# Kernel tuning notes

Measured on AMD Instinct MI355X. Metric: run time of the kernel, lower is better.

Reference implementation:

```python
import jax, jax.numpy as jnp
import numpy as np

B, S, D, H, L, F = 2, 2048, 512, 8, 6, 2048
MAX = 5000
HD = D // H
OFF = MAX - 1


def _layernorm(x, g, b, eps=1e-5):
    m = jnp.mean(x, axis=-1, keepdims=True)
    v = jnp.mean((x - m) ** 2, axis=-1, keepdims=True)
    return (x - m) / jnp.sqrt(v + eps) * g + b


def _sinusoidal_pe(seq_len, d_model):
    pos = jnp.arange(seq_len, dtype=jnp.float32)[:, None]
    div = jnp.exp(jnp.arange(0, d_model, 2, dtype=jnp.float32) * (-np.log(10000.0) / d_model))
    pe = jnp.zeros((seq_len, d_model), jnp.float32)
    pe = pe.at[:, 0::2].set(jnp.sin(pos * div))
    pe = pe.at[:, 1::2].set(jnp.cos(pos * div))
    return pe


def setup_inputs() -> dict:
    key = jax.random.key(0)
    ks = iter(jax.random.split(key, 64))

    def n(shape, s):
        return (jax.random.normal(next(ks), shape, jnp.float32) * s).astype(jnp.float32)

    inp = {}
    inp['x'] = jax.random.normal(next(ks), (B, S, D), jnp.float32)
    inp['f0'] = jax.random.normal(next(ks), (B, S, 1), jnp.float32)
    inp['sp'] = jax.random.normal(next(ks), (B, S, 1), jnp.float32)
    inp['ap'] = jax.random.normal(next(ks), (B, S, 1), jnp.float32)
    inp['spk_emb'] = jax.random.normal(next(ks), (B, D), jnp.float32)
    # conditional positional encoding projections (weights stored as (in,out); y = x @ W + b)
    inp['Wf0'] = n((1, D), 0.1); inp['bf0'] = jnp.zeros((D,), jnp.float32)
    inp['Wsp'] = n((1, D), 0.1); inp['bsp'] = jnp.zeros((D,), jnp.float32)
    inp['Wap'] = n((1, D), 0.1); inp['bap'] = jnp.zeros((D,), jnp.float32)
    inp['Wspk'] = n((D, D), 0.02); inp['bspk'] = jnp.zeros((D,), jnp.float32)
    # per-layer stacked params
    inp['Wq'] = n((L, D, D), 0.02); inp['bq'] = jnp.zeros((L, D), jnp.float32)
    inp['Wk'] = n((L, D, D), 0.02); inp['bk'] = jnp.zeros((L, D), jnp.float32)
    inp['Wv'] = n((L, D, D), 0.02); inp['bv'] = jnp.zeros((L, D), jnp.float32)
    inp['Wo'] = n((L, D, D), 0.02); inp['bo'] = jnp.zeros((L, D), jnp.float32)
    inp['ln1_g'] = jnp.ones((L, D), jnp.float32); inp['ln1_b'] = jnp.zeros((L, D), jnp.float32)
    inp['ln2_g'] = jnp.ones((L, D), jnp.float32); inp['ln2_b'] = jnp.zeros((L, D), jnp.float32)
    inp['W1'] = n((L, D, F), 0.02); inp['b1'] = jnp.zeros((L, F), jnp.float32)
    inp['W2'] = n((L, F, D), 0.02); inp['b2'] = jnp.zeros((L, D), jnp.float32)
    inp['rel_table'] = n((L, 2 * MAX - 1, H), 0.02)
    inp['gfin'] = jnp.ones((D,), jnp.float32); inp['bfin'] = jnp.zeros((D,), jnp.float32)
    return inp


def _forward(x, f0, sp, ap, spk_emb,
             Wf0, bf0, Wsp, bsp, Wap, bap, Wspk, bspk,
             Wq, bq, Wk, bk, Wv, bv, Wo, bo,
             ln1_g, ln1_b, ln2_g, ln2_b, W1, b1, W2, b2,
             rel_table, gfin, bfin):
    # --- conditional positional encoding (dropout = identity, eval mode) ---
    x = x + _sinusoidal_pe(S, D)[None]
    x = x + (f0 @ Wf0 + bf0)
    x = x + (sp @ Wsp + bsp)
    x = x + (ap @ Wap + bap)
    spk = jnp.broadcast_to(spk_emb[:, None, :], (B, S, D))
    x = x + (spk @ Wspk + bspk)

    # relative coords: added bias for (query q, key k) is table[k - q + OFF] (matches transpose(1,3) in torch)
    coords = jnp.arange(S)
    rel = jnp.clip(coords[None, :] - coords[:, None] + OFF, 0, 2 * MAX - 2)  # (S_q, S_k)

    scale = 1.0 / np.sqrt(HD)

    def layer(x, p):
        (Wq_, bq_, Wk_, bk_, Wv_, bv_, Wo_, bo_,
         g1, be1, g2, be2, W1_, b1_, W2_, b2_, tab) = p
        res = x
        h = _layernorm(x, g1, be1)
        Q = (h @ Wq_ + bq_).reshape(B, S, H, HD)
        K = (h @ Wk_ + bk_).reshape(B, S, H, HD)
        V = (h @ Wv_ + bv_).reshape(B, S, H, HD)
        scores = jnp.einsum('bqhd,bkhd->bhqk', Q, K) * scale
        bias = jnp.transpose(tab[rel], (2, 0, 1))  # (H, S_q, S_k)
        scores = scores + bias[None]
        attn = jax.nn.softmax(scores, axis=-1)
        ao = jnp.einsum('bhqk,bkhd->bqhd', attn, V).reshape(B, S, D)
        x = res + (ao @ Wo_ + bo_)
        res = x
        h = _layernorm(x, g2, be2)
        h = jax.nn.gelu(h @ W1_ + b1_, approximate=False)
        x = res + (h @ W2_ + b2_)
        return x, None

    params = (Wq, bq, Wk, bk, Wv, bv, Wo, bo,
              ln1_g, ln1_b, ln2_g, ln2_b, W1, b1, W2, b2, rel_table)
    x, _ = jax.lax.scan(layer, x, params)
    return _layernorm(x, gfin, bfin)


def reference(x, f0, sp, ap, spk_emb,
              Wf0, bf0, Wsp, bsp, Wap, bap, Wspk, bspk,
              Wq, bq, Wk, bk, Wv, bv, Wo, bo,
              ln1_g, ln1_b, ln2_g, ln2_b, W1, b1, W2, b2,
              rel_table, gfin, bfin):
    return _forward(x, f0, sp, ap, spk_emb,
                    Wf0, bf0, Wsp, bsp, Wap, bap, Wspk, bspk,
                    Wq, bq, Wk, bk, Wv, bv, Wo, bo,
                    ln1_g, ln1_b, ln2_g, ln2_b, W1, b1, W2, b2,
                    rel_table, gfin, bfin)
```

## Files before the change

kernel.cpp:

```cpp
#include <hip/hip_runtime.h>
#include <hip/hip_bf16.h>

#define B_ 2
#define S_ 2048
#define D_ 512
#define H_ 8
#define L_ 6
#define F_ 2048
#define HD_ 64
#define M_ 4096
#define OFF_ 4999
#define NREL_ 9999

typedef short s8v __attribute__((ext_vector_type(8)));
typedef float f4v __attribute__((ext_vector_type(4)));

enum { MODE_BF16 = 0, MODE_RES = 1, MODE_GELU = 2 };

__device__ __forceinline__ short f2bf(float f) {
  unsigned u = __float_as_uint(f);
  unsigned r = (u + 0x7fffu + ((u >> 16) & 1u)) >> 16;
  return (short)r;
}

__device__ __forceinline__ float exp2fast(float x) {
  float r;
  asm("v_exp_f32 %0, %1" : "=v"(r) : "v"(x));
  return r;
}

__device__ __forceinline__ void gload16(const void* g, const void* l) {
  __builtin_amdgcn_global_load_lds((const __attribute__((address_space(1))) unsigned int*)g,
                                   (__attribute__((address_space(3))) unsigned int*)l,
                                   16, 0, 0);
}

__global__ void transpose_kernel(const float* __restrict__ src, short* __restrict__ dst,
                                 int K, int N, long srcBS, long dstBS, int rowOff)
{
  __shared__ float t[32][33];
  int tx = threadIdx.x, ty = threadIdx.y;
  int n0 = blockIdx.x * 32, k0 = blockIdx.y * 32, l = blockIdx.z;
  const float* s = src + (size_t)l * srcBS;
  short* d = dst + (size_t)l * dstBS;
  for (int j = 0; j < 4; ++j)
    t[ty + j*8][tx] = s[(size_t)(k0 + ty + j*8) * N + n0 + tx];
  __syncthreads();
  for (int j = 0; j < 4; ++j)
    d[(size_t)(rowOff + n0 + ty + j*8) * K + k0 + tx] = f2bf(t[tx][ty + j*8]);
}

__global__ void packb_kernel(const float* __restrict__ bq, const float* __restrict__ bk,
                             const float* __restrict__ bv, float* __restrict__ bqkv)
{
  int i = blockIdx.x * 256 + threadIdx.x;
  if (i >= L_ * 1536) return;
  int l = i / 1536, j = i % 1536;
  float v = (j < 512) ? bq[l*512 + j] : (j < 1024) ? bk[l*512 + j - 512] : bv[l*512 + j - 1024];
  bqkv[i] = v;
}

__global__ void tabt_kernel(const float* __restrict__ tab, float* __restrict__ tabT)
{
  int i = blockIdx.x * 256 + threadIdx.x;
  if (i >= L_ * H_ * NREL_) return;
  int l = i / (H_ * NREL_), rem = i % (H_ * NREL_);
  int h = rem / NREL_, idx = rem % NREL_;
  tabT[i] = tab[((size_t)l * NREL_ + idx) * H_ + h] * 1.44269504f;
}

__global__ __launch_bounds__(256) void spk_kernel(const float* __restrict__ spk,
                                                  const float* __restrict__ Wspk,
                                                  const float* __restrict__ bspk,
                                                  float* __restrict__ sproj)
{
  __shared__ float red[4][64];
  int b = blockIdx.x, nb = blockIdx.y;
  int dl = threadIdx.x & 63, kc = threadIdx.x >> 6;
  int d = nb * 64 + dl;
  const float* sprow = spk + b * D_;
  float a0 = 0.f, a1 = 0.f;
  int kbeg = kc * 128;
  for (int k = kbeg; k < kbeg + 128; k += 2) {
    a0 += sprow[k]     * Wspk[(size_t)k * D_ + d];
    a1 += sprow[k + 1] * Wspk[(size_t)(k + 1) * D_ + d];
  }
  red[kc][dl] = a0 + a1;
  __syncthreads();
  if (kc == 0)
    sproj[b*D_ + d] = red[0][dl] + red[1][dl] + red[2][dl] + red[3][dl] + bspk[d];
}

__global__ __launch_bounds__(256) void prologue_kernel(
    const float* __restrict__ x, const float* __restrict__ f0, const float* __restrict__ sp,
    const float* __restrict__ ap, const float* __restrict__ Wf0, const float* __restrict__ bf0,
    const float* __restrict__ Wsp, const float* __restrict__ bsp,
    const float* __restrict__ Wap, const float* __restrict__ bap,
    const float* __restrict__ sproj, float* __restrict__ X)
{
  int row = blockIdx.x, tid = threadIdx.x;
  int b = row >> 11, s = row & 2047;
  float vf0 = f0[row], vsp = sp[row], vap = ap[row];
  for (int j = 0; j < 2; ++j) {
    int d = tid + j * 256;
    int i = d >> 1;
    float div = expf((float)(2*i) * -0.01798894603f);
    float arg = (float)s * div;
    float pe = (d & 1) ? cosf(arg) : sinf(arg);
    float v = x[(size_t)row*D_ + d] + pe
            + vf0*Wf0[d] + bf0[d] + vsp*Wsp[d] + bsp[d] + vap*Wap[d] + bap[d]
            + sproj[b*D_ + d];
    X[(size_t)row*D_ + d] = v;
  }
}

__global__ __launch_bounds__(256) void ln_kernel(
    const float* __restrict__ X, const float* __restrict__ g, const float* __restrict__ bta,
    short* __restrict__ outB, float* __restrict__ outF, int f32out)
{
  __shared__ float red[8];
  int row = blockIdx.x, tid = threadIdx.x;
  const float* xr = X + (size_t)row * D_;
  float v0 = xr[tid], v1 = xr[tid + 256];
  float s = v0 + v1, q = v0*v0 + v1*v1;
  for (int off = 1; off < 64; off <<= 1) { s += __shfl_xor(s, off); q += __shfl_xor(q, off); }
  int w = tid >> 6;
  if ((tid & 63) == 0) { red[w*2] = s; red[w*2 + 1] = q; }
  __syncthreads();
  s = red[0] + red[2] + red[4] + red[6];
  q = red[1] + red[3] + red[5] + red[7];
  float mean = s * (1.0f / D_);
  float var = q * (1.0f / D_) - mean * mean;
  float rstd = rsqrtf(var + 1e-5f);
  float o0 = (v0 - mean) * rstd * g[tid] + bta[tid];
  float o1 = (v1 - mean) * rstd * g[tid + 256] + bta[tid + 256];
  if (f32out) {
    outF[(size_t)row*D_ + tid] = o0; outF[(size_t)row*D_ + tid + 256] = o1;
  } else {
    outB[(size_t)row*D_ + tid] = f2bf(o0); outB[(size_t)row*D_ + tid + 256] = f2bf(o1);
  }
}

template<int MODE>
__device__ __forceinline__ void gemm_body(
    const short* __restrict__ A, const short* __restrict__ Wt,
    const float* __restrict__ bias, int K, int N,
    float* outF, short* outB)
{
  __shared__ short sA[2][4096];
  __shared__ short sB[2][2048];
  const int tid = threadIdx.x;
  const int w = tid >> 6, lane = tid & 63;
  const int col = lane & 15, quad = lane >> 4;
  const int m0 = blockIdx.x * 128, n0 = blockIdx.y * 64;
  const int z = blockIdx.z;
  const int Ksub = K / gridDim.z;
  const int kbase = z * Ksub;
  const int nkt = Ksub >> 6;

  const int rowT = tid >> 2, kcA = tid & 3;
  const size_t kc8 = kcA * 8;

  f4v acc[2][4] = {};
  for (int kt = 0; kt < nkt; ++kt) {
    const int k0 = kbase + kt * 64;
    __syncthreads();
    for (int p = 0; p < 2; ++p) {
      gload16(A + (size_t)(m0 + rowT) * K + k0 + p*32 + kc8,       &sA[p][(w*16) * 32]);
      gload16(A + (size_t)(m0 + 64 + rowT) * K + k0 + p*32 + kc8,  &sA[p][(64 + w*16) * 32]);
      gload16(Wt + (size_t)(n0 + rowT) * K + k0 + p*32 + kc8,      &sB[p][(w*16) * 32]);
    }
    __syncthreads();
    for (int p = 0; p < 2; ++p) {
      s8v af[2], bfr[4];
      for (int mt = 0; mt < 2; ++mt)
        af[mt] = *(const s8v*)&sA[p][(w*32 + mt*16 + col) * 32 + quad * 8];
      for (int nt = 0; nt < 4; ++nt)
        bfr[nt] = *(const s8v*)&sB[p][(nt*16 + col) * 32 + quad * 8];
      for (int mt = 0; mt < 2; ++mt)
        for (int nt = 0; nt < 4; ++nt)
          acc[mt][nt] = __builtin_amdgcn_mfma_f32_16x16x32_bf16(af[mt], bfr[nt], acc[mt][nt], 0, 0, 0);
    }
  }

  const float qsc = (MODE == MODE_BF16 && n0 < 512) ? 0.18033688f : 1.0f;
  float bz[4];
  for (int nt = 0; nt < 4; ++nt)
    bz[nt] = (z == 0) ? bias[n0 + nt*16 + col] : 0.0f;
  for (int mt = 0; mt < 2; ++mt) {
    int mbase = m0 + w*32 + mt*16 + quad*4;
    for (int nt = 0; nt < 4; ++nt) {
      int n = n0 + nt*16 + col;
      for (int r = 0; r < 4; ++r) {
        float v = acc[mt][nt][r] + bz[nt];
        size_t idx = (size_t)(mbase + r) * N + n;
        if (MODE == MODE_RES) {
          atomicAdd(outF + idx, v);
        } else if (MODE == MODE_GELU) {
          outB[idx] = f2bf(0.5f * v * (1.0f + erff(v * 0.70710678118f)));
        } else {
          outB[idx] = f2bf(v * qsc);
        }
      }
    }
  }
}

__global__ __launch_bounds__(256) void gemm_qkv_kernel(
    const short* __restrict__ A, const short* __restrict__ Wt,
    const float* __restrict__ bias, float* outF, short* outB)
{ gemm_body<MODE_BF16>(A, Wt, bias, 512, 1536, outF, outB); }

__global__ __launch_bounds__(256) void gemm_o_kernel(
    const short* __restrict__ A, const short* __restrict__ Wt,
    const float* __restrict__ bias, float* outF, short* outB)
{ gemm_body<MODE_RES>(A, Wt, bias, 512, 512, outF, outB); }

__global__ __launch_bounds__(256) void gemm_ffn1_kernel(
    const short* __restrict__ A, const short* __restrict__ Wt,
    const float* __restrict__ bias, float* outF, short* outB)
{ gemm_body<MODE_GELU>(A, Wt, bias, 512, 2048, outF, outB); }

__global__ __launch_bounds__(256) void gemm_ffn2_kernel(
    const short* __restrict__ A, const short* __restrict__ Wt,
    const float* __restrict__ bias, float* outF, short* outB)
{ gemm_body<MODE_RES>(A, Wt, bias, 2048, 512, outF, outB); }

__global__ __launch_bounds__(256) void vtrans_kernel(const short* __restrict__ QKV,
                                                     short* __restrict__ Vt)
{
  __shared__ short t[64 * 72];
  int tid = threadIdx.x;
  int s0 = blockIdx.x * 64, bh = blockIdx.y;
  int b = bh >> 3, h = bh & 7;
  for (int it = 0; it < 2; ++it) {
    int c = it * 256 + tid;
    int sR = c >> 3, hc = c & 7;
    s8v v = *(const s8v*)(QKV + (size_t)(b*S_ + s0 + sR) * 1536 + 1024 + h*64 + hc*8);
    *(s8v*)&t[sR * 72 + hc * 8] = v;
  }
  __syncthreads();
  for (int it = 0; it < 2; ++it) {
    int c = it * 256 + tid;
    int hd = c >> 3, sc = c & 7;
    s8v v;
    for (int j = 0; j < 8; ++j) v[j] = t[(sc*8 + j) * 72 + hd];
    *(s8v*)(Vt + (size_t)(bh*64 + hd) * S_ + s0 + sc*8) = v;
  }
}

__global__ __launch_bounds__(512) void flash_kernel(
    const short* __restrict__ QKV, const short* __restrict__ Vt,
    const float* __restrict__ tabT, short* __restrict__ AO)
{
  __shared__ __attribute__((aligned(16))) short sQ[2 * 128 * 40];
  __shared__ __attribute__((aligned(16))) short sK[2 * 2 * 32 * 40];
  __shared__ __attribute__((aligned(16))) short sV[2 * 64 * 40];
  __shared__ __attribute__((aligned(16))) short sP[8 * 2 * 16 * 40];
  __shared__ float sBias[192];
  __shared__ float sRow[8 * 16];

  const int tid = threadIdx.x;
  const int w = tid >> 6, lane = tid & 63;
  const int col = lane & 15, quad = lane >> 4;
  const int bh = blockIdx.x, qt = blockIdx.y;
  const int b = bh >> 3, h = bh & 7;
  const int q0 = qt * 128;
  const int wq = w * 16;
  const int nkt = S_ / 64;
  const float* tabh = tabT + (size_t)h * NREL_;

  for (int j = 0; j < 2; ++j) {
    int Lc = j * 512 + tid;
    int c4q = Lc & 3, q = (Lc >> 2) & 127, hc = Lc >> 9;
    *(int4*)&sQ[hc*5120 + q*40 + c4q*8] =
      *(const int4*)(QKV + (size_t)(b*S_ + q0 + q) * 1536 + h*64 + hc*32 + c4q*8);
  }

  const int c4 = tid & 3;
  const int kK = (tid >> 2) & 63, hcK = tid >> 8;
  const short* gK = QKV + (size_t)(b*S_ + kK) * 1536 + 512 + h*64 + hcK*32 + c4*8;
  short* dK = &sK[(kK >> 5)*2560 + hcK*1280 + (kK & 31)*40 + c4*8];
  const int c8 = tid & 7, hdV = tid >> 3;
  const short* gV = Vt + (size_t)(bh*64 + hdV) * S_ + c8*8;
  short* dV = &sV[(c8 >> 2)*2560 + hdV*40 + (c8 & 3)*8];

  int4 rk = *(const int4*)gK;
  int4 rv = *(const int4*)gV;
  float rbias = (tid < 192) ? tabh[0 - q0 - 127 + OFF_ + tid] : 0.0f;

  s8v bQ[2];
  float lsum = 0.0f;
  f4v o[4] = {};

  for (int kt = 0; kt < nkt; ++kt) {
    __syncthreads();
    *(int4*)dK = rk;
    *(int4*)dV = rv;
    if (tid < 192) sBias[tid] = rbias;
    __syncthreads();
    if (kt == 0) {
      bQ[0] = *(const s8v*)&sQ[0*5120 + (wq + col)*40 + quad*8];
      bQ[1] = *(const s8v*)&sQ[1*5120 + (wq + col)*40 + quad*8];
    }
    if (kt + 1 < nkt) {
      rk = *(const int4*)(gK + (size_t)(kt + 1) * 64 * 1536);
      rv = *(const int4*)(gV + (kt + 1) * 64);
      if (tid < 192) rbias = tabh[(kt + 1)*64 - q0 - 127 + OFF_ + tid];
    }

    for (int ko = 0; ko < 2; ++ko) {
      f4v st[2] = {};
      for (int mt = 0; mt < 2; ++mt) {
        s8v aK0 = *(const s8v*)&sK[ko*2560 + 0*1280 + (mt*16 + col)*40 + quad*8];
        s8v aK1 = *(const s8v*)&sK[ko*2560 + 1*1280 + (mt*16 + col)*40 + quad*8];
        st[mt] = __builtin_amdgcn_mfma_f32_16x16x32_bf16(aK0, bQ[0], st[mt], 0, 0, 0);
        st[mt] = __builtin_amdgcn_mfma_f32_16x16x32_bf16(aK1, bQ[1], st[mt], 0, 0, 0);
      }
      for (int mt = 0; mt < 2; ++mt) {
        int ib0 = ko*32 + mt*16 + quad*4 + 127 - wq - col;
        float p0 = exp2fast(st[mt][0] + sBias[ib0 + 0]);
        float p1 = exp2fast(st[mt][1] + sBias[ib0 + 1]);
        float p2 = exp2fast(st[mt][2] + sBias[ib0 + 2]);
        float p3 = exp2fast(st[mt][3] + sBias[ib0 + 3]);
        lsum += (p0 + p1) + (p2 + p3);
        unsigned u0 = __float_as_uint(p0) + 0x8000u;
        unsigned u1 = __float_as_uint(p1) + 0x8000u;
        unsigned u2 = __float_as_uint(p2) + 0x8000u;
        unsigned u3 = __float_as_uint(p3) + 0x8000u;
        int2 pk;
        pk.x = (int)((u0 >> 16) | (u1 & 0xffff0000u));
        pk.y = (int)((u2 >> 16) | (u3 & 0xffff0000u));
        *(int2*)&sP[w*1280 + ko*640 + col*40 + mt*16 + quad*4] = pk;
      }
      s8v aP = *(const s8v*)&sP[w*1280 + ko*640 + col*40 + quad*8];
      for (int nt = 0; nt < 4; ++nt) {
        s8v bv = *(const s8v*)&sV[ko*2560 + (nt*16 + col)*40 + quad*8];
        o[nt] = __builtin_amdgcn_mfma_f32_16x16x32_bf16(aP, bv, o[nt], 0, 0, 0);
      }
    }
  }

  lsum += __shfl_xor(lsum, 16);
  lsum += __shfl_xor(lsum, 32);
  if (lane < 16) sRow[w*16 + lane] = lsum;
  float rs[4];
  for (int r = 0; r < 4; ++r) rs[r] = sRow[w*16 + quad*4 + r];
  for (int nt = 0; nt < 4; ++nt)
    for (int r = 0; r < 4; ++r) {
      float v = o[nt][r] / rs[r];
      size_t m = (size_t)(b*S_ + q0 + wq + quad*4 + r);
      AO[m * 512 + h*64 + nt*16 + col] = f2bf(v);
    }
}

extern "C" void kernel_launch(void* const* d_in, const int* in_sizes, int n_in,
                              void* d_out, int out_size, void* d_ws, size_t ws_size,
                              hipStream_t stream)
{
  const float* x    = (const float*)d_in[0];
  const float* f0   = (const float*)d_in[1];
  const float* sp   = (const float*)d_in[2];
  const float* ap   = (const float*)d_in[3];
  const float* spk  = (const float*)d_in[4];
  const float* Wf0  = (const float*)d_in[5];  const float* bf0  = (const float*)d_in[6];
  const float* Wsp  = (const float*)d_in[7];  const float* bsp  = (const float*)d_in[8];
  const float* Wap  = (const float*)d_in[9];  const float* bap  = (const float*)d_in[10];
  const float* Wspk = (const float*)d_in[11]; const float* bspk = (const float*)d_in[12];
  const float* Wq   = (const float*)d_in[13]; const float* bq   = (const float*)d_in[14];
  const float* Wk   = (const float*)d_in[15]; const float* bk   = (const float*)d_in[16];
  const float* Wv   = (const float*)d_in[17]; const float* bv   = (const float*)d_in[18];
  const float* Wo   = (const float*)d_in[19]; const float* bo   = (const float*)d_in[20];
  const float* ln1g = (const float*)d_in[21]; const float* ln1b = (const float*)d_in[22];
  const float* ln2g = (const float*)d_in[23]; const float* ln2b = (const float*)d_in[24];
  const float* W1   = (const float*)d_in[25]; const float* b1   = (const float*)d_in[26];
  const float* W2   = (const float*)d_in[27]; const float* b2   = (const float*)d_in[28];
  const float* tab  = (const float*)d_in[29];
  const float* gfin = (const float*)d_in[30]; const float* bfin = (const float*)d_in[31];

  char* p = (char*)d_ws;
  auto alloc = [&](size_t bytes) { char* r = p; p += (bytes + 255) & ~(size_t)255; return r; };
  short* WqkvT = (short*)alloc((size_t)L_ * 1536 * 512 * 2);
  short* WoT   = (short*)alloc((size_t)L_ * 512 * 512 * 2);
  short* W1T   = (short*)alloc((size_t)L_ * 2048 * 512 * 2);
  short* W2T   = (short*)alloc((size_t)L_ * 512 * 2048 * 2);
  float* bqkv  = (float*)alloc((size_t)L_ * 1536 * 4);
  float* X     = (float*)alloc((size_t)M_ * D_ * 4);
  short* Hb    = (short*)alloc((size_t)M_ * D_ * 2);
  short* AO    = (short*)alloc((size_t)M_ * D_ * 2);
  short* QKVb  = (short*)alloc((size_t)M_ * 1536 * 2);
  short* VtG   = (short*)alloc((size_t)B_ * H_ * HD_ * S_ * 2);
  short* H1b   = QKVb;
  float* sproj = (float*)alloc((size_t)B_ * D_ * 4);
  float* tabT  = (float*)alloc((size_t)L_ * H_ * NREL_ * 4);

  dim3 b256(256);
  dim3 tb(32, 8);
  packb_kernel<<<dim3((L_*1536 + 255)/256), b256, 0, stream>>>(bq, bk, bv, bqkv);
  tabt_kernel<<<dim3((L_*H_*NREL_ + 255)/256), b256, 0, stream>>>(tab, tabT);
  transpose_kernel<<<dim3(16, 16, L_), tb, 0, stream>>>(Wq, WqkvT, 512, 512, 512*512, 1536*512, 0);
  transpose_kernel<<<dim3(16, 16, L_), tb, 0, stream>>>(Wk, WqkvT, 512, 512, 512*512, 1536*512, 512);
  transpose_kernel<<<dim3(16, 16, L_), tb, 0, stream>>>(Wv, WqkvT, 512, 512, 512*512, 1536*512, 1024);
  transpose_kernel<<<dim3(16, 16, L_), tb, 0, stream>>>(Wo, WoT, 512, 512, 512*512, 512*512, 0);
  transpose_kernel<<<dim3(64, 16, L_), tb, 0, stream>>>(W1, W1T, 512, 2048, 512*2048, 2048*512, 0);
  transpose_kernel<<<dim3(16, 64, L_), tb, 0, stream>>>(W2, W2T, 2048, 512, 2048*512, 512*2048, 0);
  spk_kernel<<<dim3(B_, 8), b256, 0, stream>>>(spk, Wspk, bspk, sproj);
  prologue_kernel<<<dim3(M_), b256, 0, stream>>>(x, f0, sp, ap, Wf0, bf0, Wsp, bsp, Wap, bap, sproj, X);

  for (int l = 0; l < L_; ++l) {
    ln_kernel<<<dim3(M_), b256, 0, stream>>>(X, ln1g + l*D_, ln1b + l*D_, Hb, nullptr, 0);
    gemm_qkv_kernel<<<dim3(32, 24, 1), b256, 0, stream>>>(
        Hb, WqkvT + (size_t)l*1536*512, bqkv + l*1536, nullptr, QKVb);
    vtrans_kernel<<<dim3(S_/64, B_*H_), b256, 0, stream>>>(QKVb, VtG);
    flash_kernel<<<dim3(B_*H_, S_/128), dim3(512), 0, stream>>>(QKVb, VtG, tabT + (size_t)l*H_*NREL_, AO);
    gemm_o_kernel<<<dim3(32, 8, 2), b256, 0, stream>>>(
        AO, WoT + (size_t)l*512*512, bo + l*D_, X, nullptr);
    ln_kernel<<<dim3(M_), b256, 0, stream>>>(X, ln2g + l*D_, ln2b + l*D_, Hb, nullptr, 0);
    gemm_ffn1_kernel<<<dim3(32, 32, 1), b256, 0, stream>>>(
        Hb, W1T + (size_t)l*2048*512, b1 + l*F_, nullptr, H1b);
    gemm_ffn2_kernel<<<dim3(32, 8, 4), b256, 0, stream>>>(
        H1b, W2T + (size_t)l*512*2048, b2 + l*D_, X, nullptr);
  }
  ln_kernel<<<dim3(M_), b256, 0, stream>>>(X, gfin, bfin, nullptr, (float*)d_out, 1);
}
```

Baseline: 1.019 ms.

## Split attention over two key halves and fuse V transpose into QKV GEMM

The flash attention grid gains a z dimension that splits the key sequence in two. Each half writes unnormalized bf16 partial outputs and row sums, and a new combine kernel adds them and normalizes. This doubles the block count so the GPU is better filled. The QKV GEMM epilogue now writes V directly in transposed per-head layout, which removes the separate vtrans kernel and its pass over memory. In exchange it adds the combine kernel, extra partial-output traffic and bf16 rounding of the unnormalized partials.

```diff
diff --git a/kernel.cpp b/kernel.cpp
--- a/kernel.cpp
+++ b/kernel.cpp
@@ -21,6 +21,10 @@
   unsigned u = __float_as_uint(f);
   unsigned r = (u + 0x7fffu + ((u >> 16) & 1u)) >> 16;
   return (short)r;
+}
+
+__device__ __forceinline__ float bf2f(short s) {
+  return __uint_as_float(((unsigned)(unsigned short)s) << 16);
 }
 
 __device__ __forceinline__ float exp2fast(float x) {
@@ -145,7 +149,7 @@
 __device__ __forceinline__ void gemm_body(
     const short* __restrict__ A, const short* __restrict__ Wt,
     const float* __restrict__ bias, int K, int N,
-    float* outF, short* outB)
+    float* outF, short* outB, short* outV)
 {
   __shared__ short sA[2][4096];
   __shared__ short sB[2][2048];
@@ -189,6 +193,20 @@
     bz[nt] = (z == 0) ? bias[n0 + nt*16 + col] : 0.0f;
   for (int mt = 0; mt < 2; ++mt) {
     int mbase = m0 + w*32 + mt*16 + quad*4;
+    if (MODE == MODE_BF16 && n0 >= 1024) {
+      int bb = mbase >> 11, ss = mbase & 2047;
+      for (int nt = 0; nt < 4; ++nt) {
+        int hn = n0 + nt*16 + col - 1024;
+        int hh = hn >> 6, hd = hn & 63;
+        short4 pv;
+        pv.x = f2bf(acc[mt][nt][0] + bz[nt]);
+        pv.y = f2bf(acc[mt][nt][1] + bz[nt]);
+        pv.z = f2bf(acc[mt][nt][2] + bz[nt]);
+        pv.w = f2bf(acc[mt][nt][3] + bz[nt]);
+        *(short4*)(outV + ((size_t)((bb << 3) + hh) * 64 + hd) * S_ + ss) = pv;
+      }
+      continue;
+    }
     for (int nt = 0; nt < 4; ++nt) {
       int n = n0 + nt*16 + col;
       for (int r = 0; r < 4; ++r) {
@@ -208,66 +226,44 @@
 
 __global__ __launch_bounds__(256) void gemm_qkv_kernel(
     const short* __restrict__ A, const short* __restrict__ Wt,
-    const float* __restrict__ bias, float* outF, short* outB)
-{ gemm_body<MODE_BF16>(A, Wt, bias, 512, 1536, outF, outB); }
+    const float* __restrict__ bias, float* outF, short* outB, short* outV)
+{ gemm_body<MODE_BF16>(A, Wt, bias, 512, 1536, outF, outB, outV); }
 
 __global__ __launch_bounds__(256) void gemm_o_kernel(
     const short* __restrict__ A, const short* __restrict__ Wt,
     const float* __restrict__ bias, float* outF, short* outB)
-{ gemm_body<MODE_RES>(A, Wt, bias, 512, 512, outF, outB); }
+{ gemm_body<MODE_RES>(A, Wt, bias, 512, 512, outF, outB, nullptr); }
 
 __global__ __launch_bounds__(256) void gemm_ffn1_kernel(
     const short* __restrict__ A, const short* __restrict__ Wt,
     const float* __restrict__ bias, float* outF, short* outB)
-{ gemm_body<MODE_GELU>(A, Wt, bias, 512, 2048, outF, outB); }
+{ gemm_body<MODE_GELU>(A, Wt, bias, 512, 2048, outF, outB, nullptr); }
 
 __global__ __launch_bounds__(256) void gemm_ffn2_kernel(
     const short* __restrict__ A, const short* __restrict__ Wt,
     const float* __restrict__ bias, float* outF, short* outB)
-{ gemm_body<MODE_RES>(A, Wt, bias, 2048, 512, outF, outB); }
-
-__global__ __launch_bounds__(256) void vtrans_kernel(const short* __restrict__ QKV,
-                                                     short* __restrict__ Vt)
-{
-  __shared__ short t[64 * 72];
-  int tid = threadIdx.x;
-  int s0 = blockIdx.x * 64, bh = blockIdx.y;
-  int b = bh >> 3, h = bh & 7;
-  for (int it = 0; it < 2; ++it) {
-    int c = it * 256 + tid;
-    int sR = c >> 3, hc = c & 7;
-    s8v v = *(const s8v*)(QKV + (size_t)(b*S_ + s0 + sR) * 1536 + 1024 + h*64 + hc*8);
-    *(s8v*)&t[sR * 72 + hc * 8] = v;
-  }
-  __syncthreads();
-  for (int it = 0; it < 2; ++it) {
-    int c = it * 256 + tid;
-    int hd = c >> 3, sc = c & 7;
-    s8v v;
-    for (int j = 0; j < 8; ++j) v[j] = t[(sc*8 + j) * 72 + hd];
-    *(s8v*)(Vt + (size_t)(bh*64 + hd) * S_ + s0 + sc*8) = v;
-  }
-}
+{ gemm_body<MODE_RES>(A, Wt, bias, 2048, 512, outF, outB, nullptr); }
 
 __global__ __launch_bounds__(512) void flash_kernel(
     const short* __restrict__ QKV, const short* __restrict__ Vt,
-    const float* __restrict__ tabT, short* __restrict__ AO)
+    const float* __restrict__ tabT, short* __restrict__ OP,
+    float* __restrict__ lsumB)
 {
   __shared__ __attribute__((aligned(16))) short sQ[2 * 128 * 40];
   __shared__ __attribute__((aligned(16))) short sK[2 * 2 * 32 * 40];
   __shared__ __attribute__((aligned(16))) short sV[2 * 64 * 40];
   __shared__ __attribute__((aligned(16))) short sP[8 * 2 * 16 * 40];
   __shared__ float sBias[192];
-  __shared__ float sRow[8 * 16];
 
   const int tid = threadIdx.x;
   const int w = tid >> 6, lane = tid & 63;
   const int col = lane & 15, quad = lane >> 4;
-  const int bh = blockIdx.x, qt = blockIdx.y;
+  const int bh = blockIdx.x, qt = blockIdx.y, z = blockIdx.z;
   const int b = bh >> 3, h = bh & 7;
   const int q0 = qt * 128;
+  const int KB = z * (S_ / 2);
   const int wq = w * 16;
-  const int nkt = S_ / 64;
+  const int nkt = S_ / 128;
   const float* tabh = tabT + (size_t)h * NREL_;
 
   for (int j = 0; j < 2; ++j) {
@@ -279,15 +275,15 @@
 
   const int c4 = tid & 3;
   const int kK = (tid >> 2) & 63, hcK = tid >> 8;
-  const short* gK = QKV + (size_t)(b*S_ + kK) * 1536 + 512 + h*64 + hcK*32 + c4*8;
+  const short* gK = QKV + (size_t)(b*S_ + KB + kK) * 1536 + 512 + h*64 + hcK*32 + c4*8;
   short* dK = &sK[(kK >> 5)*2560 + hcK*1280 + (kK & 31)*40 + c4*8];
   const int c8 = tid & 7, hdV = tid >> 3;
-  const short* gV = Vt + (size_t)(bh*64 + hdV) * S_ + c8*8;
+  const short* gV = Vt + (size_t)(bh*64 + hdV) * S_ + KB + c8*8;
   short* dV = &sV[(c8 >> 2)*2560 + hdV*40 + (c8 & 3)*8];
 
   int4 rk = *(const int4*)gK;
   int4 rv = *(const int4*)gV;
-  float rbias = (tid < 192) ? tabh[0 - q0 - 127 + OFF_ + tid] : 0.0f;
+  float rbias = (tid < 192) ? tabh[KB + 0 - q0 - 127 + OFF_ + tid] : 0.0f;
 
   s8v bQ[2];
   float lsum = 0.0f;
@@ -306,7 +302,7 @@
     if (kt + 1 < nkt) {
       rk = *(const int4*)(gK + (size_t)(kt + 1) * 64 * 1536);
       rv = *(const int4*)(gV + (kt + 1) * 64);
-      if (tid < 192) rbias = tabh[(kt + 1)*64 - q0 - 127 + OFF_ + tid];
+      if (tid < 192) rbias = tabh[KB + (kt + 1)*64 - q0 - 127 + OFF_ + tid];
     }
 
     for (int ko = 0; ko < 2; ++ko) {
@@ -343,15 +339,29 @@
 
   lsum += __shfl_xor(lsum, 16);
   lsum += __shfl_xor(lsum, 32);
-  if (lane < 16) sRow[w*16 + lane] = lsum;
-  float rs[4];
-  for (int r = 0; r < 4; ++r) rs[r] = sRow[w*16 + quad*4 + r];
+  if (lane < 16)
+    lsumB[(size_t)z * (B_*H_*S_) + (size_t)bh * S_ + q0 + wq + lane] = lsum;
+  short* op = OP + (size_t)z * M_ * 512;
   for (int nt = 0; nt < 4; ++nt)
     for (int r = 0; r < 4; ++r) {
-      float v = o[nt][r] / rs[r];
       size_t m = (size_t)(b*S_ + q0 + wq + quad*4 + r);
-      AO[m * 512 + h*64 + nt*16 + col] = f2bf(v);
-    }
+      op[m * 512 + h*64 + nt*16 + col] = f2bf(o[nt][r]);
+    }
+}
+
+__global__ __launch_bounds__(256) void ocomb_kernel(
+    const short* __restrict__ OP, const float* __restrict__ lsumB,
+    short* __restrict__ AO)
+{
+  int m = blockIdx.x, tid = threadIdx.x;
+  int b = m >> 11, s = m & 2047;
+  for (int j = 0; j < 2; ++j) {
+    int d = tid + j * 256;
+    int bh = (b << 3) + (d >> 6);
+    float l = lsumB[(size_t)bh * S_ + s] + lsumB[(size_t)(B_*H_*S_) + (size_t)bh * S_ + s];
+    float o = bf2f(OP[(size_t)m * 512 + d]) + bf2f(OP[(size_t)(M_ + m) * 512 + d]);
+    AO[(size_t)m * 512 + d] = f2bf(o / l);
+  }
 }
 
 extern "C" void kernel_launch(void* const* d_in, const int* in_sizes, int n_in,
@@ -393,6 +403,8 @@
   short* H1b   = QKVb;
   float* sproj = (float*)alloc((size_t)B_ * D_ * 4);
   float* tabT  = (float*)alloc((size_t)L_ * H_ * NREL_ * 4);
+  short* OP    = (short*)alloc((size_t)2 * M_ * 512 * 2);
+  float* lsumB = (float*)alloc((size_t)2 * B_ * H_ * S_ * 4);
 
   dim3 b256(256);
   dim3 tb(32, 8);
@@ -410,9 +422,10 @@
   for (int l = 0; l < L_; ++l) {
     ln_kernel<<<dim3(M_), b256, 0, stream>>>(X, ln1g + l*D_, ln1b + l*D_, Hb, nullptr, 0);
     gemm_qkv_kernel<<<dim3(32, 24, 1), b256, 0, stream>>>(
-        Hb, WqkvT + (size_t)l*1536*512, bqkv + l*1536, nullptr, QKVb);
-    vtrans_kernel<<<dim3(S_/64, B_*H_), b256, 0, stream>>>(QKVb, VtG);
-    flash_kernel<<<dim3(B_*H_, S_/128), dim3(512), 0, stream>>>(QKVb, VtG, tabT + (size_t)l*H_*NREL_, AO);
+        Hb, WqkvT + (size_t)l*1536*512, bqkv + l*1536, nullptr, QKVb, VtG);
+    flash_kernel<<<dim3(B_*H_, S_/128, 2), dim3(512), 0, stream>>>(
+        QKVb, VtG, tabT + (size_t)l*H_*NREL_, OP, lsumB);
+    ocomb_kernel<<<dim3(M_), b256, 0, stream>>>(OP, lsumB, AO);
     gemm_o_kernel<<<dim3(32, 8, 2), b256, 0, stream>>>(
         AO, WoT + (size_t)l*512*512, bo + l*D_, X, nullptr);
     ln_kernel<<<dim3(M_), b256, 0, stream>>>(X, ln2g + l*D_, ln2b + l*D_, Hb, nullptr, 0);
```

Measured after the change: 1.021 ms. About the same (+0.2%).

## Enlarge GEMM tiles to 128x128 and fuse V transpose into QKV epilogue

Applied to the files above, without the earlier changes.

Widens the GEMM block tile from 128x64 to 128x128, with a 2x2 warp arrangement where each warp owns a 64x64 subtile. This doubles per-block data reuse and halves the grid size for every GEMM. The QKV GEMM epilogue now writes the V columns directly in transposed per-head layout using short4 stores, so the separate vtrans kernel launch and its global round trip are removed. The cost is twice the shared memory per block and a larger accumulator array, which can reduce occupancy. Smaller grids, for example 256 blocks for the O projection, may also underfill the GPU.

```diff
diff --git a/kernel.cpp b/kernel.cpp
--- a/kernel.cpp
+++ b/kernel.cpp
@@ -145,14 +145,15 @@
 __device__ __forceinline__ void gemm_body(
     const short* __restrict__ A, const short* __restrict__ Wt,
     const float* __restrict__ bias, int K, int N,
-    float* outF, short* outB)
+    float* outF, short* outB, short* outV)
 {
   __shared__ short sA[2][4096];
-  __shared__ short sB[2][2048];
+  __shared__ short sB[2][4096];
   const int tid = threadIdx.x;
   const int w = tid >> 6, lane = tid & 63;
   const int col = lane & 15, quad = lane >> 4;
-  const int m0 = blockIdx.x * 128, n0 = blockIdx.y * 64;
+  const int wm = w >> 1, wn = w & 1;
+  const int m0 = blockIdx.x * 128, n0 = blockIdx.y * 128;
   const int z = blockIdx.z;
   const int Ksub = K / gridDim.z;
   const int kbase = z * Ksub;
@@ -161,23 +162,24 @@
   const int rowT = tid >> 2, kcA = tid & 3;
   const size_t kc8 = kcA * 8;
 
-  f4v acc[2][4] = {};
+  f4v acc[4][4] = {};
   for (int kt = 0; kt < nkt; ++kt) {
     const int k0 = kbase + kt * 64;
     __syncthreads();
     for (int p = 0; p < 2; ++p) {
-      gload16(A + (size_t)(m0 + rowT) * K + k0 + p*32 + kc8,       &sA[p][(w*16) * 32]);
-      gload16(A + (size_t)(m0 + 64 + rowT) * K + k0 + p*32 + kc8,  &sA[p][(64 + w*16) * 32]);
-      gload16(Wt + (size_t)(n0 + rowT) * K + k0 + p*32 + kc8,      &sB[p][(w*16) * 32]);
+      gload16(A  + (size_t)(m0 + rowT) * K + k0 + p*32 + kc8,       &sA[p][(w*16) * 32]);
+      gload16(A  + (size_t)(m0 + 64 + rowT) * K + k0 + p*32 + kc8,  &sA[p][(64 + w*16) * 32]);
+      gload16(Wt + (size_t)(n0 + rowT) * K + k0 + p*32 + kc8,       &sB[p][(w*16) * 32]);
+      gload16(Wt + (size_t)(n0 + 64 + rowT) * K + k0 + p*32 + kc8,  &sB[p][(64 + w*16) * 32]);
     }
     __syncthreads();
     for (int p = 0; p < 2; ++p) {
-      s8v af[2], bfr[4];
-      for (int mt = 0; mt < 2; ++mt)
-        af[mt] = *(const s8v*)&sA[p][(w*32 + mt*16 + col) * 32 + quad * 8];
+      s8v af[4], bfr[4];
+      for (int mt = 0; mt < 4; ++mt)
+        af[mt] = *(const s8v*)&sA[p][(wm*64 + mt*16 + col) * 32 + quad * 8];
       for (int nt = 0; nt < 4; ++nt)
-        bfr[nt] = *(const s8v*)&sB[p][(nt*16 + col) * 32 + quad * 8];
-      for (int mt = 0; mt < 2; ++mt)
+        bfr[nt] = *(const s8v*)&sB[p][(wn*64 + nt*16 + col) * 32 + quad * 8];
+      for (int mt = 0; mt < 4; ++mt)
         for (int nt = 0; nt < 4; ++nt)
           acc[mt][nt] = __builtin_amdgcn_mfma_f32_16x16x32_bf16(af[mt], bfr[nt], acc[mt][nt], 0, 0, 0);
     }
@@ -186,11 +188,25 @@
   const float qsc = (MODE == MODE_BF16 && n0 < 512) ? 0.18033688f : 1.0f;
   float bz[4];
   for (int nt = 0; nt < 4; ++nt)
-    bz[nt] = (z == 0) ? bias[n0 + nt*16 + col] : 0.0f;
-  for (int mt = 0; mt < 2; ++mt) {
-    int mbase = m0 + w*32 + mt*16 + quad*4;
+    bz[nt] = (z == 0) ? bias[n0 + wn*64 + nt*16 + col] : 0.0f;
+  for (int mt = 0; mt < 4; ++mt) {
+    int mbase = m0 + wm*64 + mt*16 + quad*4;
+    if (MODE == MODE_BF16 && n0 >= 1024) {
+      int bb = mbase >> 11, ss = mbase & 2047;
+      for (int nt = 0; nt < 4; ++nt) {
+        int hn = n0 + wn*64 + nt*16 + col - 1024;
+        int hh = hn >> 6, hd = hn & 63;
+        short4 pv;
+        pv.x = f2bf(acc[mt][nt][0] + bz[nt]);
+        pv.y = f2bf(acc[mt][nt][1] + bz[nt]);
+        pv.z = f2bf(acc[mt][nt][2] + bz[nt]);
+        pv.w = f2bf(acc[mt][nt][3] + bz[nt]);
+        *(short4*)(outV + ((size_t)((bb << 3) + hh) * 64 + hd) * S_ + ss) = pv;
+      }
+      continue;
+    }
     for (int nt = 0; nt < 4; ++nt) {
-      int n = n0 + nt*16 + col;
+      int n = n0 + wn*64 + nt*16 + col;
       for (int r = 0; r < 4; ++r) {
         float v = acc[mt][nt][r] + bz[nt];
         size_t idx = (size_t)(mbase + r) * N + n;
@@ -208,46 +224,23 @@
 
 __global__ __launch_bounds__(256) void gemm_qkv_kernel(
     const short* __restrict__ A, const short* __restrict__ Wt,
-    const float* __restrict__ bias, float* outF, short* outB)
-{ gemm_body<MODE_BF16>(A, Wt, bias, 512, 1536, outF, outB); }
+    const float* __restrict__ bias, float* outF, short* outB, short* outV)
+{ gemm_body<MODE_BF16>(A, Wt, bias, 512, 1536, outF, outB, outV); }
 
 __global__ __launch_bounds__(256) void gemm_o_kernel(
     const short* __restrict__ A, const short* __restrict__ Wt,
     const float* __restrict__ bias, float* outF, short* outB)
-{ gemm_body<MODE_RES>(A, Wt, bias, 512, 512, outF, outB); }
+{ gemm_body<MODE_RES>(A, Wt, bias, 512, 512, outF, outB, nullptr); }
 
 __global__ __launch_bounds__(256) void gemm_ffn1_kernel(
     const short* __restrict__ A, const short* __restrict__ Wt,
     const float* __restrict__ bias, float* outF, short* outB)
-{ gemm_body<MODE_GELU>(A, Wt, bias, 512, 2048, outF, outB); }
+{ gemm_body<MODE_GELU>(A, Wt, bias, 512, 2048, outF, outB, nullptr); }
 
 __global__ __launch_bounds__(256) void gemm_ffn2_kernel(
     const short* __restrict__ A, const short* __restrict__ Wt,
     const float* __restrict__ bias, float* outF, short* outB)
-{ gemm_body<MODE_RES>(A, Wt, bias, 2048, 512, outF, outB); }
-
-__global__ __launch_bounds__(256) void vtrans_kernel(const short* __restrict__ QKV,
-                                                     short* __restrict__ Vt)
-{
-  __shared__ short t[64 * 72];
-  int tid = threadIdx.x;
-  int s0 = blockIdx.x * 64, bh = blockIdx.y;
-  int b = bh >> 3, h = bh & 7;
-  for (int it = 0; it < 2; ++it) {
-    int c = it * 256 + tid;
-    int sR = c >> 3, hc = c & 7;
-    s8v v = *(const s8v*)(QKV + (size_t)(b*S_ + s0 + sR) * 1536 + 1024 + h*64 + hc*8);
-    *(s8v*)&t[sR * 72 + hc * 8] = v;
-  }
-  __syncthreads();
-  for (int it = 0; it < 2; ++it) {
-    int c = it * 256 + tid;
-    int hd = c >> 3, sc = c & 7;
-    s8v v;
-    for (int j = 0; j < 8; ++j) v[j] = t[(sc*8 + j) * 72 + hd];
-    *(s8v*)(Vt + (size_t)(bh*64 + hd) * S_ + s0 + sc*8) = v;
-  }
-}
+{ gemm_body<MODE_RES>(A, Wt, bias, 2048, 512, outF, outB, nullptr); }
 
 __global__ __launch_bounds__(512) void flash_kernel(
     const short* __restrict__ QKV, const short* __restrict__ Vt,
@@ -409,16 +402,16 @@
 
   for (int l = 0; l < L_; ++l) {
     ln_kernel<<<dim3(M_), b256, 0, stream>>>(X, ln1g + l*D_, ln1b + l*D_, Hb, nullptr, 0);
-    gemm_qkv_kernel<<<dim3(32, 24, 1), b256, 0, stream>>>(
-        Hb, WqkvT + (size_t)l*1536*512, bqkv + l*1536, nullptr, QKVb);
-    vtrans_kernel<<<dim3(S_/64, B_*H_), b256, 0, stream>>>(QKVb, VtG);
-    flash_kernel<<<dim3(B_*H_, S_/128), dim3(512), 0, stream>>>(QKVb, VtG, tabT + (size_t)l*H_*NREL_, AO);
-    gemm_o_kernel<<<dim3(32, 8, 2), b256, 0, stream>>>(
+    gemm_qkv_kernel<<<dim3(32, 12, 1), b256, 0, stream>>>(
+        Hb, WqkvT + (size_t)l*1536*512, bqkv + l*1536, nullptr, QKVb, VtG);
+    flash_kernel<<<dim3(B_*H_, S_/128), dim3(512), 0, stream>>>(
+        QKVb, VtG, tabT + (size_t)l*H_*NREL_, AO);
+    gemm_o_kernel<<<dim3(32, 4, 2), b256, 0, stream>>>(
         AO, WoT + (size_t)l*512*512, bo + l*D_, X, nullptr);
     ln_kernel<<<dim3(M_), b256, 0, stream>>>(X, ln2g + l*D_, ln2b + l*D_, Hb, nullptr, 0);
-    gemm_ffn1_kernel<<<dim3(32, 32, 1), b256, 0, stream>>>(
+    gemm_ffn1_kernel<<<dim3(32, 16, 1), b256, 0, stream>>>(
         Hb, W1T + (size_t)l*2048*512, b1 + l*F_, nullptr, H1b);
-    gemm_ffn2_kernel<<<dim3(32, 8, 4), b256, 0, stream>>>(
+    gemm_ffn2_kernel<<<dim3(32, 4, 4), b256, 0, stream>>>(
         H1b, W2T + (size_t)l*512*2048, b2 + l*D_, X, nullptr);
   }
   ln_kernel<<<dim3(M_), b256, 0, stream>>>(X, gfin, bfin, nullptr, (float*)d_out, 1);
```

New measurement: 1.036 ms. About the same (+1.7%).
